# Kernel optimization log

Hardware: AMD Instinct MI355X
Metric: run time of the kernel (lower is better)

Reference implementation:

```python
import jax, jax.numpy as jnp
import numpy as np

K = 20
EPS = 1e-5

def leaky(y):
    return jnp.where(y > 0, y, 0.2 * y)

def knn(x, k):
    # x: [B, C, N] -> idx [B, N, k] of nearest neighbors (incl. self)
    xx = jnp.sum(x * x, axis=1)                      # [B, N]
    inner = jnp.einsum('bcn,bcm->bnm', x, x)          # [B, N, N]
    pd = -xx[:, :, None] + 2.0 * inner - xx[:, None, :]  # negative sq dist
    return jax.lax.top_k(pd, k)[1]

def get_graph_feature(x, k):
    # x: [B, C, N] -> [B, 2C, N, k]
    idx = knn(x, k)
    xt = jnp.transpose(x, (0, 2, 1))                  # [B, N, C]
    feat = jax.vmap(lambda xb, ib: xb[ib])(xt, idx)   # [B, N, k, C]
    center = xt[:, :, None, :]
    out = jnp.concatenate([feat - center, jnp.broadcast_to(center, feat.shape)], axis=-1)
    return jnp.transpose(out, (0, 3, 1, 2))

def bn(y, g, b, axes, shape):
    m = jnp.mean(y, axis=axes, keepdims=True)
    v = jnp.var(y, axis=axes, keepdims=True)
    return (y - m) * jax.lax.rsqrt(v + EPS) * g.reshape(shape) + b.reshape(shape)

def edge_block(x, W, g, b, k):
    f = get_graph_feature(x, k)                       # [B, 2C, N, k]
    y = jnp.einsum('bcnk,oc->bonk', f, W)             # 1x1 conv2d, no bias
    y = leaky(bn(y, g, b, (0, 2, 3), (1, -1, 1, 1)))
    return jnp.max(y, axis=-1)                        # [B, O, N]

def setup_inputs():
    key = jax.random.key(0)
    ks = jax.random.split(key, 8)
    d = {
        'x':  jax.random.normal(ks[0], (16, 3, 2048), jnp.float32),
        'W1': jax.random.normal(ks[1], (64, 6), jnp.float32) * 0.1,
        'g1': jnp.ones((64,)), 'b1': jnp.zeros((64,)),
        'W2': jax.random.normal(ks[2], (64, 128), jnp.float32) * 0.1,
        'g2': jnp.ones((64,)), 'b2': jnp.zeros((64,)),
        'W3': jax.random.normal(ks[3], (128, 128), jnp.float32) * 0.1,
        'g3': jnp.ones((128,)), 'b3': jnp.zeros((128,)),
        'W4': jax.random.normal(ks[4], (256, 256), jnp.float32) * 0.1,
        'g4': jnp.ones((256,)), 'b4': jnp.zeros((256,)),
        'W5': jax.random.normal(ks[5], (1024, 512), jnp.float32) * 0.05,
        'g5': jnp.ones((1024,)), 'b5': jnp.zeros((1024,)),
        'Wl': jax.random.normal(ks[6], (256, 2048), jnp.float32) * 0.02,
        'g6': jnp.ones((256,)), 'b6': jnp.zeros((256,)),
    }
    return d

def reference(x, W1, g1, b1, W2, g2, b2, W3, g3, b3, W4, g4, b4, W5, g5, b5, Wl, g6, b6):
    x1 = edge_block(x,  W1, g1, b1, K)   # [B, 64, N]
    x2 = edge_block(x1, W2, g2, b2, K)   # [B, 64, N]
    x3 = edge_block(x2, W3, g3, b3, K)   # [B, 128, N]
    x4 = edge_block(x3, W4, g4, b4, K)   # [B, 256, N]
    h = jnp.concatenate([x1, x2, x3, x4], axis=1)       # [B, 512, N]
    y = jnp.einsum('bcn,oc->bon', h, W5)                 # 1x1 conv1d
    y = leaky(bn(y, g5, b5, (0, 2), (1, -1, 1)))         # [B, 1024, N]
    p = jnp.concatenate([jnp.max(y, axis=-1), jnp.mean(y, axis=-1)], axis=1)  # [B, 2048]
    z = p @ Wl.T                                          # [B, 256]
    return bn(z, g6, b6, (0,), (1, -1))
```

## Files before the change

kernel.cpp:

```cpp
#include <hip/hip_runtime.h>
#include <float.h>
#include <math.h>

#define BB 16
#define NN 2048
#define KNNK 20
#define HC 512
#define O5 1024
#define EPSF 1e-5f
#define GBLK 2048

typedef short bf16x8 __attribute__((ext_vector_type(8)));
typedef float f32x4 __attribute__((ext_vector_type(4)));

__device__ __forceinline__ float leakyf(float y){ return y > 0.f ? y : 0.2f*y; }

__device__ __forceinline__ ushort f2bf(float f){
  unsigned u = __float_as_uint(f);
  unsigned r = (u + 0x7fffu + ((u >> 16) & 1u)) >> 16;
  return (ushort)r;
}

__device__ __forceinline__ void bsort_step(float& v, int& id, int lane, int k, int j){
  float pv = __shfl_xor(v, j, 64);
  int pid = __shfl_xor(id, j, 64);
  bool up = ((lane & k) == 0);
  bool iLow = ((lane & j) == 0);
  bool pBefore = (pv > v) || (pv == v && pid < id);
  if ((up == iLow) ? pBefore : !pBefore){ v = pv; id = pid; }
}

__global__ void k_transpose(const float* __restrict__ x, float* __restrict__ xP){
  int gid = blockIdx.x*256 + threadIdx.x;
  if (gid >= BB*NN) return;
  int b = gid / NN, n = gid % NN;
  const float* xb = x + (size_t)b*3*NN;
  *(float4*)&xP[(size_t)gid*4] = make_float4(xb[n], xb[NN + n], xb[2*NN + n], 0.f);
}

__global__ void k_sqn(const float* __restrict__ xin, int xs, int C, float* __restrict__ sqn){
  int gid = blockIdx.x*256 + threadIdx.x;
  if (gid >= BB*NN) return;
  const float* r = xin + (size_t)gid*xs;
  float s = 0.f;
  for (int c = 0; c < C; ++c){ float v = r[c]; s = fmaf(v, v, s); }
  sqn[gid] = s;
}

template<int C, bool WARM>
__global__ __launch_bounds__(256) void k_knn(const float* __restrict__ xin, int xs,
                                             const float* __restrict__ sqn,
                                             const int* __restrict__ idx_prev,
                                             int* __restrict__ idx_out){
  const int TN = 16, MC = 256;
  __shared__ float xnT[WARM ? 1 : 8][20];
  __shared__ float xmT[(C == 3 ? 1 : 16)][MC + 4];
  __shared__ float cval[TN][24];
  __shared__ int   cidx[TN][24];
  __shared__ float sqnn[TN];
  int tid = threadIdx.x;
  int b = (blockIdx.x*TN) / NN, n0 = (blockIdx.x*TN) % NN;
  const float* xb = xin + (size_t)b*NN*xs;

  if constexpr (!WARM){
    for (int e = tid; e < TN*C; e += 256){
      int r = e / C, c = e % C;
      xnT[c][r] = xb[(size_t)(n0+r)*xs + c];
    }
  }
  if (tid < TN) sqnn[tid] = sqn[b*NN + n0 + tid];
  __syncthreads();

  int wid = tid >> 6, lane = tid & 63, r0 = wid*4;
  float tv[4]; int ti[4];

  int urow[4];
  #pragma unroll
  for (int i = 0; i < 4; ++i) urow[i] = __builtin_amdgcn_readfirstlane(n0 + r0 + i);

  if constexpr (WARM){
    #pragma unroll
    for (int i = 0; i < 4; ++i){
      int r = r0 + i;
      int m = (lane < KNNK) ? idx_prev[(size_t)(b*NN + n0 + r)*KNNK + lane] : 0;
      const float* xq = xb + (size_t)urow[i]*xs;
      const float* xm = xb + (size_t)m*xs;
      float dot = 0.f;
      #pragma unroll 8
      for (int c = 0; c < C; c += 4){
        float4 qv = *(const float4*)(xq + c);
        float4 mv = *(const float4*)(xm + c);
        dot = fmaf(qv.x, mv.x, dot);
        dot = fmaf(qv.y, mv.y, dot);
        dot = fmaf(qv.z, mv.z, dot);
        dot = fmaf(qv.w, mv.w, dot);
      }
      float dval = (lane < KNNK) ? ((2.f*dot - sqnn[r]) - sqn[b*NN + m]) : -FLT_MAX;
      int did = (lane < KNNK) ? m : 0x7fffffff;
      #pragma unroll
      for (int k = 2; k <= 64; k <<= 1)
        #pragma unroll
        for (int jj = k >> 1; jj > 0; jj >>= 1)
          bsort_step(dval, did, lane, k, jj);
      if (lane < KNNK){ cval[r][lane] = dval; cidx[r][lane] = did; }
      tv[i] = __shfl(dval, KNNK-1); ti[i] = __shfl(did, KNNK-1);
    }
    __syncthreads();
  }

  for (int base = 0; base < NN; base += MC){
    float pd[4][4];
    if constexpr (C == 3){
      int m0g = base + lane*4;
      const float* xm = xb + (size_t)m0g*4;
      float4 q0 = *(const float4*)&xm[0];
      float4 q1 = *(const float4*)&xm[4];
      float4 q2 = *(const float4*)&xm[8];
      float4 q3 = *(const float4*)&xm[12];
      float4 sm4 = *(const float4*)&sqn[b*NN + m0g];
      #pragma unroll
      for (int i = 0; i < 4; ++i){
        float a0 = xnT[0][r0+i], a1 = xnT[1][r0+i], a2 = xnT[2][r0+i], sq = sqnn[r0+i];
        float d0 = a0*q0.x; d0 = fmaf(a1, q0.y, d0); d0 = fmaf(a2, q0.z, d0);
        float d1 = a0*q1.x; d1 = fmaf(a1, q1.y, d1); d1 = fmaf(a2, q1.z, d1);
        float d2 = a0*q2.x; d2 = fmaf(a1, q2.y, d2); d2 = fmaf(a2, q2.z, d2);
        float d3 = a0*q3.x; d3 = fmaf(a1, q3.y, d3); d3 = fmaf(a2, q3.z, d3);
        pd[i][0] = (2.f*d0 - sq) - sm4.x;
        pd[i][1] = (2.f*d1 - sq) - sm4.y;
        pd[i][2] = (2.f*d2 - sq) - sm4.z;
        pd[i][3] = (2.f*d3 - sq) - sm4.w;
      }
    } else {
      float acc[4][4] = {};
      const float* xq0 = xb + (size_t)urow[0]*xs;
      const float* xq1 = xb + (size_t)urow[1]*xs;
      const float* xq2 = xb + (size_t)urow[2]*xs;
      const float* xq3 = xb + (size_t)urow[3]*xs;
      int pm = tid >> 2, fq = tid & 3;
      for (int c0 = 0; c0 < C; c0 += 16){
        #pragma unroll
        for (int p = 0; p < 4; ++p){
          int pt = p*64 + pm;
          float4 vv = *(const float4*)(xb + (size_t)(base + pt)*xs + c0 + fq*4);
          xmT[fq*4+0][pt] = vv.x; xmT[fq*4+1][pt] = vv.y;
          xmT[fq*4+2][pt] = vv.z; xmT[fq*4+3][pt] = vv.w;
        }
        __syncthreads();
        #pragma unroll
        for (int cc4 = 0; cc4 < 16; cc4 += 4){
          float aq[4][4];
          *(float4*)&aq[0][0] = *(const float4*)(xq0 + c0 + cc4);
          *(float4*)&aq[1][0] = *(const float4*)(xq1 + c0 + cc4);
          *(float4*)&aq[2][0] = *(const float4*)(xq2 + c0 + cc4);
          *(float4*)&aq[3][0] = *(const float4*)(xq3 + c0 + cc4);
          #pragma unroll
          for (int dc = 0; dc < 4; ++dc){
            float4 m4 = *(const float4*)&xmT[cc4+dc][lane*4];
            float mv[4] = {m4.x, m4.y, m4.z, m4.w};
            #pragma unroll
            for (int i = 0; i < 4; ++i)
              #pragma unroll
              for (int p = 0; p < 4; ++p)
                acc[i][p] = fmaf(aq[i][dc], mv[p], acc[i][p]);
          }
        }
        __syncthreads();
      }
      float4 sm4 = *(const float4*)&sqn[b*NN + base + lane*4];
      float smr[4] = {sm4.x, sm4.y, sm4.z, sm4.w};
      #pragma unroll
      for (int i = 0; i < 4; ++i){
        float sq = sqnn[r0+i];
        #pragma unroll
        for (int j = 0; j < 4; ++j)
          pd[i][j] = (2.f*acc[i][j] - sq) - smr[j];
      }
    }

    bool handled = false;
    if constexpr (!WARM){
      if (base == 0){
        handled = true;
        float lv[4]; int li[4];
        #pragma unroll
        for (int i = 0; i < 4; ++i){
          float v0 = pd[i][0]; int j0 = 0;
          if (pd[i][1] > v0){ v0 = pd[i][1]; j0 = 1; }
          if (pd[i][2] > v0){ v0 = pd[i][2]; j0 = 2; }
          if (pd[i][3] > v0){ v0 = pd[i][3]; j0 = 3; }
          lv[i] = v0; li[i] = lane*4 + j0;
        }
        float bv[4]; int bi[4];
        for (int it = 0; it < KNNK; ++it){
          #pragma unroll
          for (int i = 0; i < 4; ++i){ bv[i] = lv[i]; bi[i] = li[i]; }
          #pragma unroll
          for (int off = 1; off < 64; off <<= 1){
            #pragma unroll
            for (int i = 0; i < 4; ++i){
              float ov = __shfl_xor(bv[i], off, 64);
              int oi = __shfl_xor(bi[i], off, 64);
              if (ov > bv[i] || (ov == bv[i] && oi < bi[i])){ bv[i] = ov; bi[i] = oi; }
            }
          }
          #pragma unroll
          for (int i = 0; i < 4; ++i){
            if (lane == it){ cval[r0+i][it] = bv[i]; cidx[r0+i][it] = bi[i]; }
            int wl = bi[i] >> 2, wj = bi[i] & 3;
            if (lane == wl){
              pd[i][0] = (wj == 0) ? -FLT_MAX : pd[i][0];
              pd[i][1] = (wj == 1) ? -FLT_MAX : pd[i][1];
              pd[i][2] = (wj == 2) ? -FLT_MAX : pd[i][2];
              pd[i][3] = (wj == 3) ? -FLT_MAX : pd[i][3];
              float v0 = pd[i][0]; int j0 = 0;
              if (pd[i][1] > v0){ v0 = pd[i][1]; j0 = 1; }
              if (pd[i][2] > v0){ v0 = pd[i][2]; j0 = 2; }
              if (pd[i][3] > v0){ v0 = pd[i][3]; j0 = 3; }
              lv[i] = v0; li[i] = lane*4 + j0;
            }
          }
        }
        #pragma unroll
        for (int i = 0; i < 4; ++i){ tv[i] = bv[i]; ti[i] = bi[i]; }
      }
    }
    if (!handled){
      #pragma unroll
      for (int i = 0; i < 4; ++i){
        int r = r0 + i;
        bool pred = false;
        #pragma unroll
        for (int j = 0; j < 4; ++j){
          int ci = base + lane*4 + j;
          pred = pred || (pd[i][j] > tv[i]) || (pd[i][j] == tv[i] && ci < ti[i]);
        }
        unsigned long long mask = __ballot(pred);
        while (mask){
          int l = __builtin_ctzll(mask); mask &= (mask - 1);
          float cv0 = __shfl(pd[i][0], l);
          float cv1 = __shfl(pd[i][1], l);
          float cv2 = __shfl(pd[i][2], l);
          float cv3 = __shfl(pd[i][3], l);
          #pragma unroll
          for (int j = 0; j < 4; ++j){
            float cv = (j == 0) ? cv0 : (j == 1) ? cv1 : (j == 2) ? cv2 : cv3;
            int ci = base + l*4 + j;
            if (cv > tv[i] || (cv == tv[i] && ci < ti[i])){
              bool skip = false;
              if constexpr (WARM){
                skip = __ballot((lane < KNNK) && (cidx[r][lane] == ci)) != 0ull;
              }
              if (!skip){
                float ev = -FLT_MAX; int ei = 0x7fffffff;
                if (lane < KNNK){ ev = cval[r][lane]; ei = cidx[r][lane]; }
                bool ahead = (lane < KNNK) && (ev > cv || (ev == cv && ei < ci));
                int pos = __popcll(__ballot(ahead));
                float pev = __shfl_up(ev, 1);
                int   pei = __shfl_up(ei, 1);
                float nv; int ni;
                if (lane < pos){ nv = ev; ni = ei; }
                else if (lane == pos){ nv = cv; ni = ci; }
                else { nv = pev; ni = pei; }
                if (lane < KNNK){ cval[r][lane] = nv; cidx[r][lane] = ni; }
                tv[i] = __shfl(nv, 19); ti[i] = __shfl(ni, 19);
              }
            }
          }
        }
      }
    }
  }

  if (lane < KNNK){
    #pragma unroll
    for (int i = 0; i < 4; ++i){
      int r = r0 + i;
      idx_out[(size_t)(b*NN + n0 + r)*KNNK + lane] = cidx[r][lane];
    }
  }
}

__global__ void k_wprep(const float* __restrict__ W, int O, int C,
                        float* __restrict__ wu, float* __restrict__ wv){
  int i = blockIdx.x*256 + threadIdx.x;
  if (i >= O*C) return;
  int o = i / C, c = i % C;
  float a = W[(size_t)o*2*C + c], b = W[(size_t)o*2*C + C + c];
  wu[i] = a; wv[i] = b - a;
}

__global__ __launch_bounds__(256) void k_uv(const float* __restrict__ xin, int xs, int C,
                                            const float* __restrict__ wu, const float* __restrict__ wv,
                                            int O, float* __restrict__ u, float* __restrict__ v){
  __shared__ float xsh[16][68];
  __shared__ float wush[16][68], wvsh[16][68];
  int tid = threadIdx.x;
  int rb = blockIdx.x*64, ob = blockIdx.y*64;
  int otx = tid % 16, rty = tid / 16;
  float au[4][4] = {}, av[4][4] = {};
  for (int c0 = 0; c0 < C; c0 += 16){
    #pragma unroll
    for (int i = 0; i < 4; ++i){
      int c = otx, r = rty*4 + i;
      xsh[c][r]  = (c0 + c < C) ? xin[(size_t)(rb+r)*xs + c0 + c] : 0.f;
      wush[c][r] = (c0 + c < C) ? wu[(size_t)(ob+r)*C + c0 + c] : 0.f;
      wvsh[c][r] = (c0 + c < C) ? wv[(size_t)(ob+r)*C + c0 + c] : 0.f;
    }
    __syncthreads();
    #pragma unroll
    for (int c = 0; c < 16; ++c){
      float4 xr = *(const float4*)&xsh[c][rty*4];
      float4 wa = *(const float4*)&wush[c][otx*4];
      float4 wb = *(const float4*)&wvsh[c][otx*4];
      float xv[4] = {xr.x, xr.y, xr.z, xr.w};
      float wav[4] = {wa.x, wa.y, wa.z, wa.w};
      float wbv[4] = {wb.x, wb.y, wb.z, wb.w};
      #pragma unroll
      for (int i = 0; i < 4; ++i)
        #pragma unroll
        for (int j = 0; j < 4; ++j){
          au[i][j] = fmaf(xv[i], wav[j], au[i][j]);
          av[i][j] = fmaf(xv[i], wbv[j], av[i][j]);
        }
    }
    __syncthreads();
  }
  #pragma unroll
  for (int i = 0; i < 4; ++i){
    size_t r = (size_t)(rb + rty*4 + i);
    *(float4*)&u[r*O + ob + otx*4] = make_float4(au[i][0], au[i][1], au[i][2], au[i][3]);
    *(float4*)&v[r*O + ob + otx*4] = make_float4(av[i][0], av[i][1], av[i][2], av[i][3]);
  }
}

__global__ __launch_bounds__(256) void k_gather(const float* __restrict__ u, const float* __restrict__ v,
                                                const int* __restrict__ idx, int O,
                                                float* __restrict__ s,
                                                float* __restrict__ gp1, float* __restrict__ gp2){
  __shared__ float r1[256], r2[256];
  int tid = threadIdx.x;
  int Ppar = 256 / O;
  int o = tid % O, g = tid / O;
  int p0 = blockIdx.x*16;
  float cs = 0.f, cs2 = 0.f;
  int IT = 16 / Ppar;
  for (int it = 0; it < IT; ++it){
    int pi = p0 + it*Ppar + g;
    int b = pi / NN;
    const int* il = idx + (size_t)pi*KNNK;
    float vv = v[(size_t)pi*O + o];
    float mx = -FLT_MAX, su = 0.f, su2 = 0.f;
    #pragma unroll
    for (int k = 0; k < KNNK; ++k){
      int m = il[k];
      float um = u[((size_t)b*NN + m)*O + o];
      mx = fmaxf(mx, um); su += um; su2 = fmaf(um, um, su2);
    }
    s[(size_t)pi*O + o] = mx + vv;
    cs += su + (float)KNNK*vv;
    cs2 += su2 + 2.f*vv*su + (float)KNNK*vv*vv;
  }
  r1[tid] = cs; r2[tid] = cs2;
  __syncthreads();
  if (tid < O){
    float t1 = 0.f, t2 = 0.f;
    for (int gg = 0; gg < Ppar; ++gg){ t1 += r1[gg*O + tid]; t2 += r2[gg*O + tid]; }
    gp1[(size_t)tid*GBLK + blockIdx.x] = t1;
    gp2[(size_t)tid*GBLK + blockIdx.x] = t2;
  }
}

__global__ __launch_bounds__(256) void k_pred(const float* __restrict__ gp1, const float* __restrict__ gp2,
                                              float* __restrict__ S1, float* __restrict__ S2){
  __shared__ float r1[256], r2[256];
  int o = blockIdx.x, t = threadIdx.x;
  float a = 0.f, b = 0.f;
  #pragma unroll
  for (int i = 0; i < GBLK/256; ++i){
    a += gp1[(size_t)o*GBLK + i*256 + t];
    b += gp2[(size_t)o*GBLK + i*256 + t];
  }
  r1[t] = a; r2[t] = b;
  __syncthreads();
  for (int off = 128; off > 0; off >>= 1){
    if (t < off){ r1[t] += r1[t + off]; r2[t] += r2[t + off]; }
    __syncthreads();
  }
  if (t == 0){ S1[o] = r1[0]; S2[o] = r2[0]; }
}

__global__ void k_fin(const float* __restrict__ S1, const float* __restrict__ S2,
                      const float* __restrict__ g, const float* __restrict__ bb,
                      int O, float cnt, float* __restrict__ A, float* __restrict__ Bp){
  int o = blockIdx.x*256 + threadIdx.x;
  if (o >= O) return;
  float m = S1[o] / cnt;
  float var = S2[o] / cnt - m*m;
  float sc = g[o] / sqrtf(var + EPSF);
  A[o] = sc; Bp[o] = bb[o] - m*sc;
}

__global__ void k_bnle(const float* __restrict__ s, const float* __restrict__ A,
                       const float* __restrict__ Bp, int O, int choff, float* __restrict__ h){
  int gid = blockIdx.x*256 + threadIdx.x;
  int row = gid / O, o = gid % O;
  h[(size_t)row*HC + choff + o] = leakyf(fmaf(s[gid], A[o], Bp[o]));
}

__global__ void k_h2bf(const float* __restrict__ h, ushort* __restrict__ hbf){
  int gid = blockIdx.x*256 + threadIdx.x;
  float4 v = *(const float4*)&h[(size_t)gid*4];
  ushort4 o;
  o.x = f2bf(v.x); o.y = f2bf(v.y); o.z = f2bf(v.z); o.w = f2bf(v.w);
  *(ushort4*)&hbf[(size_t)gid*4] = o;
}

__global__ void k_w5cvt(const float* __restrict__ W5, ushort* __restrict__ w5bf){
  int gid = blockIdx.x*256 + threadIdx.x;
  float4 v = *(const float4*)&W5[(size_t)gid*4];
  ushort4 o;
  o.x = f2bf(v.x); o.y = f2bf(v.y); o.z = f2bf(v.z); o.w = f2bf(v.w);
  *(ushort4*)&w5bf[(size_t)gid*4] = o;
}

__global__ void k_colsum(const float* __restrict__ hh, float* __restrict__ cp){
  __shared__ float red[4][64];
  int c = threadIdx.x & 63, g = threadIdx.x >> 6;
  int cb = blockIdx.x*64;
  int rbase = blockIdx.y*2048;
  float sacc = 0.f;
  for (int r = rbase + g; r < rbase + 2048; r += 4)
    sacc += hh[(size_t)r*HC + cb + c];
  red[g][c] = sacc;
  __syncthreads();
  if (threadIdx.x < 64){
    float t = red[0][c] + red[1][c] + red[2][c] + red[3][c];
    cp[(size_t)blockIdx.y*HC + cb + c] = t;
  }
}

__global__ void k_csred(const float* __restrict__ cp, float* __restrict__ cs){
  int c = blockIdx.x*256 + threadIdx.x;
  if (c >= HC) return;
  float s = 0.f;
  for (int g = 0; g < 16; ++g) s += cp[(size_t)g*HC + c];
  cs[c] = s;
}

__global__ __launch_bounds__(256) void k_syrk(const float* __restrict__ hh, float* __restrict__ Gp){
  __shared__ float as[16][132], bs[16][132];
  int tid = threadIdx.x;
  int ib = blockIdx.x*128, jb = blockIdx.y*128;
  int k0 = blockIdx.z*1024;
  int cx = tid & 15, ry = tid >> 4;
  int skk = tid >> 4, scc = (tid & 15)*8;
  float acc[8][8] = {};
  for (int kk0 = k0; kk0 < k0 + 1024; kk0 += 16){
    {
      const float* ra = &hh[(size_t)(kk0 + skk)*HC + ib + scc];
      const float* rb2 = &hh[(size_t)(kk0 + skk)*HC + jb + scc];
      float4 a0 = *(const float4*)ra, a1 = *(const float4*)(ra + 4);
      float4 b0 = *(const float4*)rb2, b1 = *(const float4*)(rb2 + 4);
      *(float4*)&as[skk][scc] = a0; *(float4*)&as[skk][scc+4] = a1;
      *(float4*)&bs[skk][scc] = b0; *(float4*)&bs[skk][scc+4] = b1;
    }
    __syncthreads();
    #pragma unroll
    for (int kk = 0; kk < 16; ++kk){
      float4 a0 = *(const float4*)&as[kk][ry*8];
      float4 a1 = *(const float4*)&as[kk][ry*8+4];
      float4 b0 = *(const float4*)&bs[kk][cx*8];
      float4 b1 = *(const float4*)&bs[kk][cx*8+4];
      float av[8] = {a0.x,a0.y,a0.z,a0.w,a1.x,a1.y,a1.z,a1.w};
      float bv[8] = {b0.x,b0.y,b0.z,b0.w,b1.x,b1.y,b1.z,b1.w};
      #pragma unroll
      for (int i = 0; i < 8; ++i)
        #pragma unroll
        for (int j = 0; j < 8; ++j)
          acc[i][j] = fmaf(av[i], bv[j], acc[i][j]);
    }
    __syncthreads();
  }
  float* gz = Gp + (size_t)blockIdx.z*HC*HC;
  #pragma unroll
  for (int i = 0; i < 8; ++i){
    size_t row = (size_t)(ib + ry*8 + i);
    *(float4*)&gz[row*HC + jb + cx*8]     = make_float4(acc[i][0], acc[i][1], acc[i][2], acc[i][3]);
    *(float4*)&gz[row*HC + jb + cx*8 + 4] = make_float4(acc[i][4], acc[i][5], acc[i][6], acc[i][7]);
  }
}

__global__ void k_gred(const float* __restrict__ Gp, float* __restrict__ G){
  int e = blockIdx.x*256 + threadIdx.x;
  float s = 0.f;
  for (int z = 0; z < 32; ++z) s += Gp[(size_t)z*HC*HC + e];
  G[e] = s;
}

__global__ __launch_bounds__(256) void k_quad(const float* __restrict__ G, const float* __restrict__ W5,
                                              const float* __restrict__ cs,
                                              float* __restrict__ S1, float* __restrict__ S2){
  __shared__ float wsh[512];
  __shared__ float red[256];
  int o = blockIdx.x, tid = threadIdx.x;
  for (int j = tid; j < 512; j += 256) wsh[j] = W5[(size_t)o*HC + j];
  __syncthreads();
  float q = 0.f;
  for (int i = tid; i < 512; i += 256){
    float wi = wsh[i];
    float rd = 0.f;
    for (int j = 0; j < 512; j += 4){
      float4 gv = *(const float4*)&G[(size_t)i*HC + j];
      rd = fmaf(gv.x, wsh[j], rd); rd = fmaf(gv.y, wsh[j+1], rd);
      rd = fmaf(gv.z, wsh[j+2], rd); rd = fmaf(gv.w, wsh[j+3], rd);
    }
    q = fmaf(wi, rd, q);
  }
  float m = 0.f;
  for (int j = tid; j < 512; j += 256) m = fmaf(wsh[j], cs[j], m);
  red[tid] = q; __syncthreads();
  for (int off = 128; off > 0; off >>= 1){ if (tid < off) red[tid] += red[tid + off]; __syncthreads(); }
  if (tid == 0) S2[o] = red[0];
  __syncthreads();
  red[tid] = m; __syncthreads();
  for (int off = 128; off > 0; off >>= 1){ if (tid < off) red[tid] += red[tid + off]; __syncthreads(); }
  if (tid == 0) S1[o] = red[0];
}

__global__ __launch_bounds__(256) void k_gemm5m(const ushort* __restrict__ hbf, const ushort* __restrict__ w5bf,
                                                const float* __restrict__ A, const float* __restrict__ Bp,
                                                float* __restrict__ mpart, float* __restrict__ spart){
  __shared__ ushort lh[128][40];
  __shared__ ushort lw[128][40];
  __shared__ float redm[4][128], reds[4][128];
  int tid = threadIdx.x;
  int rb = blockIdx.x*128, ob = blockIdx.y*128;
  int wid = tid >> 6, lane = tid & 63;
  int lrow = lane & 15, lk = lane >> 4;
  f32x4 acc[2][8];
  #pragma unroll
  for (int i = 0; i < 2; ++i)
    #pragma unroll
    for (int j = 0; j < 8; ++j)
      acc[i][j] = (f32x4){0.f, 0.f, 0.f, 0.f};
  int srow = tid >> 1, shalf = tid & 1;
  for (int kt = 0; kt < 16; ++kt){
    int k0 = kt*32;
    const uint4* gh = (const uint4*)&hbf[(size_t)(rb+srow)*HC + k0 + shalf*16];
    uint4 v0 = gh[0], v1 = gh[1];
    const uint4* gw = (const uint4*)&w5bf[(size_t)(ob+srow)*HC + k0 + shalf*16];
    uint4 w0 = gw[0], w1 = gw[1];
    __syncthreads();
    *(uint4*)&lh[srow][shalf*16]     = v0;
    *(uint4*)&lh[srow][shalf*16 + 8] = v1;
    *(uint4*)&lw[srow][shalf*16]     = w0;
    *(uint4*)&lw[srow][shalf*16 + 8] = w1;
    __syncthreads();
    bf16x8 afr0 = *(const bf16x8*)&lh[wid*32 + lrow][lk*8];
    bf16x8 afr1 = *(const bf16x8*)&lh[wid*32 + 16 + lrow][lk*8];
    #pragma unroll
    for (int ct = 0; ct < 8; ++ct){
      bf16x8 bfr = *(const bf16x8*)&lw[ct*16 + lrow][lk*8];
      acc[0][ct] = __builtin_amdgcn_mfma_f32_16x16x32_bf16(afr0, bfr, acc[0][ct], 0, 0, 0);
      acc[1][ct] = __builtin_amdgcn_mfma_f32_16x16x32_bf16(afr1, bfr, acc[1][ct], 0, 0, 0);
    }
  }
  float mx[8], sm[8];
  #pragma unroll
  for (int ct = 0; ct < 8; ++ct){
    int o = ob + ct*16 + lrow;
    float Ao = A[o], Bo = Bp[o];
    float m = -FLT_MAX, s = 0.f;
    #pragma unroll
    for (int tA = 0; tA < 2; ++tA)
      #pragma unroll
      for (int q = 0; q < 4; ++q){
        float y = leakyf(fmaf(acc[tA][ct][q], Ao, Bo));
        m = fmaxf(m, y); s += y;
      }
    #pragma unroll
    for (int off = 16; off < 64; off <<= 1){
      m = fmaxf(m, __shfl_xor(m, off, 64));
      s += __shfl_xor(s, off, 64);
    }
    mx[ct] = m; sm[ct] = s;
  }
  __syncthreads();
  if (lane < 16){
    #pragma unroll
    for (int ct = 0; ct < 8; ++ct){
      redm[wid][ct*16 + lane] = mx[ct];
      reds[wid][ct*16 + lane] = sm[ct];
    }
  }
  __syncthreads();
  if (tid < 128){
    float m = fmaxf(fmaxf(redm[0][tid], redm[1][tid]), fmaxf(redm[2][tid], redm[3][tid]));
    float s = reds[0][tid] + reds[1][tid] + reds[2][tid] + reds[3][tid];
    int bbi = rb / NN, ntile = (rb % NN) >> 7;
    int o = ob + tid;
    mpart[((size_t)bbi*O5 + o)*16 + ntile] = m;
    spart[((size_t)bbi*O5 + o)*16 + ntile] = s;
  }
}

__global__ void k_pool(const float* __restrict__ mpart, const float* __restrict__ spart,
                       float* __restrict__ p){
  int gid = blockIdx.x*256 + threadIdx.x;
  if (gid >= BB*O5) return;
  int b = gid / O5, o = gid % O5;
  const float* mp = mpart + (size_t)(b*O5 + o)*16;
  const float* sp = spart + (size_t)(b*O5 + o)*16;
  float mx = -FLT_MAX, sm = 0.f;
  for (int t = 0; t < 16; ++t){ mx = fmaxf(mx, mp[t]); sm += sp[t]; }
  p[(size_t)b*2048 + o] = mx;
  p[(size_t)b*2048 + 1024 + o] = sm * (1.f/2048.f);
}

__global__ __launch_bounds__(256) void k_final(const float* __restrict__ p, const float* __restrict__ Wl,
                                               const float* __restrict__ g6, const float* __restrict__ b6,
                                               float* __restrict__ out){
  __shared__ float red[16][257];
  int oc = blockIdx.x, tid = threadIdx.x;
  float acc[16] = {};
  for (int j = tid; j < 2048; j += 256){
    float w = Wl[(size_t)oc*2048 + j];
    #pragma unroll
    for (int b = 0; b < 16; ++b) acc[b] = fmaf(p[(size_t)b*2048 + j], w, acc[b]);
  }
  #pragma unroll
  for (int b = 0; b < 16; ++b) red[b][tid] = acc[b];
  __syncthreads();
  for (int off = 128; off > 0; off >>= 1){
    if (tid < off){
      #pragma unroll
      for (int b = 0; b < 16; ++b) red[b][tid] += red[b][tid + off];
    }
    __syncthreads();
  }
  if (tid == 0){
    float m = 0.f;
    for (int b = 0; b < 16; ++b) m += red[b][0];
    m *= (1.f/16.f);
    float var = 0.f;
    for (int b = 0; b < 16; ++b){ float d = red[b][0] - m; var = fmaf(d, d, var); }
    var *= (1.f/16.f);
    float sc = g6[oc] / sqrtf(var + EPSF);
    for (int b = 0; b < 16; ++b) out[(size_t)b*256 + oc] = (red[b][0] - m)*sc + b6[oc];
  }
}

extern "C" void kernel_launch(void* const* d_in, const int* in_sizes, int n_in,
                              void* d_out, int out_size, void* d_ws, size_t ws_size,
                              hipStream_t stream){
  const float* x  = (const float*)d_in[0];
  const float* W1 = (const float*)d_in[1];  const float* g1 = (const float*)d_in[2];  const float* b1 = (const float*)d_in[3];
  const float* W2 = (const float*)d_in[4];  const float* g2 = (const float*)d_in[5];  const float* b2 = (const float*)d_in[6];
  const float* W3 = (const float*)d_in[7];  const float* g3 = (const float*)d_in[8];  const float* b3 = (const float*)d_in[9];
  const float* W4 = (const float*)d_in[10]; const float* g4 = (const float*)d_in[11]; const float* b4 = (const float*)d_in[12];
  const float* W5 = (const float*)d_in[13]; const float* g5 = (const float*)d_in[14]; const float* b5 = (const float*)d_in[15];
  const float* Wl = (const float*)d_in[16]; const float* g6 = (const float*)d_in[17]; const float* b6 = (const float*)d_in[18];
  float* out = (float*)d_out;

  float* ws = (float*)d_ws;
  size_t off = 0;
  auto alloc = [&](size_t n){ float* pp = ws + off; off += n; return pp; };
  float* h    = alloc((size_t)BB*NN*HC);
  float* u    = alloc((size_t)BB*NN*256);
  float* v    = alloc((size_t)BB*NN*256);
  float* s    = alloc((size_t)BB*NN*256);
  float* xP   = alloc((size_t)BB*NN*4);
  float* sqn  = alloc((size_t)BB*NN);
  int*   idxA = (int*)alloc((size_t)BB*NN*KNNK);
  int*   idxB = (int*)alloc((size_t)BB*NN*KNNK);
  float* wu   = alloc(256*128);
  float* wv   = alloc(256*128);
  float* S1   = alloc(1024);
  float* S2   = alloc(1024);
  float* Ab   = alloc(1024);
  float* Bb   = alloc(1024);
  float* mpart= alloc((size_t)BB*O5*16);
  float* spart= alloc((size_t)BB*O5*16);
  float* pbuf = alloc((size_t)BB*2048);
  float* G    = alloc((size_t)HC*HC);
  float* cs   = alloc(HC);
  float* cp   = alloc((size_t)16*HC);
  float* gp1  = alloc((size_t)256*GBLK);
  float* gp2  = alloc((size_t)256*GBLK);
  ushort* w5bf = (ushort*)alloc(262144);
  float* Gp   = u;
  ushort* hbf = (ushort*)s;

  k_transpose<<<(BB*NN)/256, 256, 0, stream>>>(x, xP);

  struct Cfg { const float* xin; int xs, C, O, choff; const float* W; const float* g; const float* bb; };
  Cfg cfg[4] = {
    { xP,    4,   3,   64,   0, W1, g1, b1 },
    { h,     HC,  64,  64,  64, W2, g2, b2 },
    { h+64,  HC,  64, 128, 128, W3, g3, b3 },
    { h+128, HC, 128, 256, 256, W4, g4, b4 },
  };

  int* cur = idxA;
  int* prv = idxB;
  for (int i = 0; i < 4; ++i){
    const Cfg& c = cfg[i];
    k_sqn<<<(BB*NN)/256, 256, 0, stream>>>(c.xin, c.xs, c.C, sqn);
    if (i == 0)           k_knn<3,false><<<(BB*NN)/16, 256, 0, stream>>>(c.xin, c.xs, sqn, nullptr, cur);
    else if (c.C == 64)   k_knn<64,true><<<(BB*NN)/16, 256, 0, stream>>>(c.xin, c.xs, sqn, prv, cur);
    else                  k_knn<128,true><<<(BB*NN)/16, 256, 0, stream>>>(c.xin, c.xs, sqn, prv, cur);
    int OC = c.O * c.C;
    k_wprep<<<(OC + 255)/256, 256, 0, stream>>>(c.W, c.O, c.C, wu, wv);
    k_uv<<<dim3((BB*NN)/64, c.O/64), 256, 0, stream>>>(c.xin, c.xs, c.C, wu, wv, c.O, u, v);
    k_gather<<<GBLK, 256, 0, stream>>>(u, v, cur, c.O, s, gp1, gp2);
    k_pred<<<c.O, 256, 0, stream>>>(gp1, gp2, S1, S2);
    k_fin<<<4, 256, 0, stream>>>(S1, S2, c.g, c.bb, c.O, (float)((size_t)BB*NN*KNNK), Ab, Bb);
    k_bnle<<<((size_t)BB*NN*c.O)/256, 256, 0, stream>>>(s, Ab, Bb, c.O, c.choff, h);
    int* t = cur; cur = prv; prv = t;
  }

  k_h2bf<<<((size_t)BB*NN*HC)/(256*4), 256, 0, stream>>>(h, hbf);
  k_w5cvt<<<((size_t)O5*HC)/(256*4), 256, 0, stream>>>(W5, w5bf);

  k_colsum<<<dim3(8, 16), 256, 0, stream>>>(h, cp);
  k_csred<<<2, 256, 0, stream>>>(cp, cs);
  k_syrk<<<dim3(4, 4, 32), 256, 0, stream>>>(h, Gp);
  k_gred<<<(HC*HC)/256, 256, 0, stream>>>(Gp, G);
  k_quad<<<O5, 256, 0, stream>>>(G, W5, cs, S1, S2);
  k_fin<<<4, 256, 0, stream>>>(S1, S2, g5, b5, O5, (float)((size_t)BB*NN), Ab, Bb);
  k_gemm5m<<<dim3((BB*NN)/128, O5/128), 256, 0, stream>>>(hbf, w5bf, Ab, Bb, mpart, spart);
  k_pool<<<(BB*O5)/256, 256, 0, stream>>>(mpart, spart, pbuf);

  k_final<<<256, 256, 0, stream>>>(pbuf, Wl, g6, b6, out);
}
```

Before: 2.134 ms.

## Pre-transpose features to channel-major so kNN reads candidates directly from global memory

Adds a tiled transpose kernel that writes each layer's features in [B, C, N] layout before the warm kNN pass. The kNN distance loop then loads candidate columns as coalesced float4 reads straight from global memory. This replaces the per-tile shared-memory staging and its two block barriers per 16 channels. It costs an extra transpose launch and a 16 MB scratch buffer, and relies on L2/cache hits for the candidate rows that every block re-reads.

```diff
diff --git a/kernel.cpp b/kernel.cpp
--- a/kernel.cpp
+++ b/kernel.cpp
@@ -38,6 +38,21 @@
   *(float4*)&xP[(size_t)gid*4] = make_float4(xb[n], xb[NN + n], xb[2*NN + n], 0.f);
 }
 
+__global__ void k_xpose(const float* __restrict__ xin, int C, float* __restrict__ xT){
+  __shared__ float t[32][33];
+  int n0 = blockIdx.x*32, c0 = blockIdx.y*32, b = blockIdx.z;
+  int lx = threadIdx.x & 31, ly = threadIdx.x >> 5;
+  const float* src = xin + (size_t)b*NN*HC;
+  #pragma unroll
+  for (int i = 0; i < 32; i += 8)
+    t[ly+i][lx] = src[(size_t)(n0+ly+i)*HC + c0 + lx];
+  __syncthreads();
+  float* dst = xT + (size_t)b*C*NN;
+  #pragma unroll
+  for (int i = 0; i < 32; i += 8)
+    dst[(size_t)(c0+ly+i)*NN + n0 + lx] = t[lx][ly+i];
+}
+
 __global__ void k_sqn(const float* __restrict__ xin, int xs, int C, float* __restrict__ sqn){
   int gid = blockIdx.x*256 + threadIdx.x;
   if (gid >= BB*NN) return;
@@ -51,10 +66,10 @@
 __global__ __launch_bounds__(256) void k_knn(const float* __restrict__ xin, int xs,
                                              const float* __restrict__ sqn,
                                              const int* __restrict__ idx_prev,
+                                             const float* __restrict__ xT,
                                              int* __restrict__ idx_out){
   const int TN = 16, MC = 256;
   __shared__ float xnT[WARM ? 1 : 8][20];
-  __shared__ float xmT[(C == 3 ? 1 : 16)][MC + 4];
   __shared__ float cval[TN][24];
   __shared__ int   cidx[TN][24];
   __shared__ float sqnn[TN];
@@ -107,6 +122,8 @@
     }
     __syncthreads();
   }
+
+  const float* xTb = WARM ? (xT + (size_t)b*C*NN) : nullptr;
 
   for (int base = 0; base < NN; base += MC){
     float pd[4][4];
@@ -136,35 +153,24 @@
       const float* xq1 = xb + (size_t)urow[1]*xs;
       const float* xq2 = xb + (size_t)urow[2]*xs;
       const float* xq3 = xb + (size_t)urow[3]*xs;
-      int pm = tid >> 2, fq = tid & 3;
-      for (int c0 = 0; c0 < C; c0 += 16){
+      const float* xm0 = xTb + base + lane*4;
+      #pragma unroll 4
+      for (int c0 = 0; c0 < C; c0 += 4){
+        float aq[4][4];
+        *(float4*)&aq[0][0] = *(const float4*)(xq0 + c0);
+        *(float4*)&aq[1][0] = *(const float4*)(xq1 + c0);
+        *(float4*)&aq[2][0] = *(const float4*)(xq2 + c0);
+        *(float4*)&aq[3][0] = *(const float4*)(xq3 + c0);
         #pragma unroll
-        for (int p = 0; p < 4; ++p){
-          int pt = p*64 + pm;
-          float4 vv = *(const float4*)(xb + (size_t)(base + pt)*xs + c0 + fq*4);
-          xmT[fq*4+0][pt] = vv.x; xmT[fq*4+1][pt] = vv.y;
-          xmT[fq*4+2][pt] = vv.z; xmT[fq*4+3][pt] = vv.w;
+        for (int dc = 0; dc < 4; ++dc){
+          float4 m4 = *(const float4*)(xm0 + (size_t)(c0+dc)*NN);
+          float mv[4] = {m4.x, m4.y, m4.z, m4.w};
+          #pragma unroll
+          for (int i = 0; i < 4; ++i)
+            #pragma unroll
+            for (int p = 0; p < 4; ++p)
+              acc[i][p] = fmaf(aq[i][dc], mv[p], acc[i][p]);
         }
-        __syncthreads();
-        #pragma unroll
-        for (int cc4 = 0; cc4 < 16; cc4 += 4){
-          float aq[4][4];
-          *(float4*)&aq[0][0] = *(const float4*)(xq0 + c0 + cc4);
-          *(float4*)&aq[1][0] = *(const float4*)(xq1 + c0 + cc4);
-          *(float4*)&aq[2][0] = *(const float4*)(xq2 + c0 + cc4);
-          *(float4*)&aq[3][0] = *(const float4*)(xq3 + c0 + cc4);
-          #pragma unroll
-          for (int dc = 0; dc < 4; ++dc){
-            float4 m4 = *(const float4*)&xmT[cc4+dc][lane*4];
-            float mv[4] = {m4.x, m4.y, m4.z, m4.w};
-            #pragma unroll
-            for (int i = 0; i < 4; ++i)
-              #pragma unroll
-              for (int p = 0; p < 4; ++p)
-                acc[i][p] = fmaf(aq[i][dc], mv[p], acc[i][p]);
-          }
-        }
-        __syncthreads();
       }
       float4 sm4 = *(const float4*)&sqn[b*NN + base + lane*4];
       float smr[4] = {sm4.x, sm4.y, sm4.z, sm4.w};
@@ -688,6 +694,7 @@
   float* gp1  = alloc((size_t)256*GBLK);
   float* gp2  = alloc((size_t)256*GBLK);
   ushort* w5bf = (ushort*)alloc(262144);
+  float* xT   = alloc((size_t)BB*128*NN);
   float* Gp   = u;
   ushort* hbf = (ushort*)s;
 
@@ -706,9 +713,13 @@
   for (int i = 0; i < 4; ++i){
     const Cfg& c = cfg[i];
     k_sqn<<<(BB*NN)/256, 256, 0, stream>>>(c.xin, c.xs, c.C, sqn);
-    if (i == 0)           k_knn<3,false><<<(BB*NN)/16, 256, 0, stream>>>(c.xin, c.xs, sqn, nullptr, cur);
-    else if (c.C == 64)   k_knn<64,true><<<(BB*NN)/16, 256, 0, stream>>>(c.xin, c.xs, sqn, prv, cur);
-    else                  k_knn<128,true><<<(BB*NN)/16, 256, 0, stream>>>(c.xin, c.xs, sqn, prv, cur);
+    if (i == 0){
+      k_knn<3,false><<<(BB*NN)/16, 256, 0, stream>>>(c.xin, c.xs, sqn, nullptr, nullptr, cur);
+    } else {
+      k_xpose<<<dim3(NN/32, c.C/32, BB), 256, 0, stream>>>(c.xin, c.C, xT);
+      if (c.C == 64) k_knn<64,true><<<(BB*NN)/16, 256, 0, stream>>>(c.xin, c.xs, sqn, prv, xT, cur);
+      else           k_knn<128,true><<<(BB*NN)/16, 256, 0, stream>>>(c.xin, c.xs, sqn, prv, xT, cur);
+    }
     int OC = c.O * c.C;
     k_wprep<<<(OC + 255)/256, 256, 0, stream>>>(c.W, c.O, c.C, wu, wv);
     k_uv<<<dim3((BB*NN)/64, c.O/64), 256, 0, stream>>>(c.xin, c.xs, c.C, wu, wv, c.O, u, v);
```

Result: no change. 2.156 ms (+1.0%).
